# Optimization experiments

Hardware: AMD Instinct MI355X
Metric: run time of the kernel (lower is better)

The kernel has to match this reference:

```python
import jax, jax.numpy as jnp
import numpy as np

O_DIM, A_DIM, Z_DIM = 256, 8, 9
D, H, L, M, B = 128, 128, 4, 4, 65536  # module dim, MLP hidden, n_layers, n_modules, batch


def setup_inputs() -> dict:
    key = jax.random.key(0)
    ks = jax.random.split(key, 18)
    s = 0.05
    return {
        "o": jax.random.normal(ks[0], (B, O_DIM), jnp.float32),
        "z_map": jax.random.uniform(ks[1], (B, Z_DIM), jnp.float32),
        "collision_prob": jax.random.uniform(ks[2], (B, 1), jnp.float32),
        # base obs embedding and routing (task) embedding
        "Wb": jax.random.normal(ks[3], (O_DIM, D), jnp.float32) * s,
        "bb": jnp.zeros((D,), jnp.float32),
        "Wz": jax.random.normal(ks[4], (Z_DIM + 1, D), jnp.float32) * s,
        "bz": jnp.zeros((D,), jnp.float32),
        # L layers x M modules of DxD linears
        "Wm": jax.random.normal(ks[5], (L, M, D, D), jnp.float32) * s,
        "bm": jnp.zeros((L, M, D), jnp.float32),
        # routing heads: L-1 inter-layer (M*M) gates + final (M,) gate
        "Wg": jax.random.normal(ks[6], (L - 1, D, M * M), jnp.float32) * s,
        "Wg_last": jax.random.normal(ks[7], (D, M), jnp.float32) * s,
        # dueling heads
        "Wv": jax.random.normal(ks[8], (D, 1), jnp.float32) * s,
        "bv": jnp.zeros((1,), jnp.float32),
        "Wa1": jax.random.normal(ks[9], (D, H), jnp.float32) * s,
        "ba1": jnp.zeros((H,), jnp.float32),
        "Wa2": jax.random.normal(ks[10], (H, A_DIM), jnp.float32) * s,
        "ba2": jnp.zeros((A_DIM,), jnp.float32),
    }


def _softmodule(o, z_map, collision_prob, Wb, bb, Wz, bz, Wm, bm, Wg, Wg_last):
    f0 = jax.nn.relu(o @ Wb + bb)                              # (B, D)
    z_in = jnp.concatenate([z_map, collision_prob], axis=-1)   # (B, Z+1)
    g = jax.nn.relu(z_in @ Wz + bz) * f0                       # routing embedding (B, D)
    # layer 0: all modules consume the obs embedding
    x = jax.nn.relu(jnp.einsum("bd,mde->bme", f0, Wm[0]) + bm[0])  # (B, M, D)
    for l in range(1, L):
        logits = (g @ Wg[l - 1]).reshape(-1, M, M)             # (B, i, j)
        p = jax.nn.softmax(logits, axis=1)                     # soft routing over incoming modules i
        xin = jnp.einsum("bij,bid->bjd", p, x)                 # weighted gather-combine
        x = jax.nn.relu(jnp.einsum("bmd,mde->bme", xin, Wm[l]) + bm[l])
    p_last = jax.nn.softmax(g @ Wg_last, axis=-1)              # (B, M)
    return jnp.einsum("bm,bmd->bd", p_last, x)                 # (B, D)


def reference(o, z_map, collision_prob, Wb, bb, Wz, bz, Wm, bm, Wg, Wg_last,
              Wv, bv, Wa1, ba1, Wa2, ba2):
    feature = _softmodule(o, z_map, collision_prob, Wb, bb, Wz, bz, Wm, bm, Wg, Wg_last)
    value = feature @ Wv + bv                                  # (B, 1)
    adv = jax.nn.relu(feature @ Wa1 + ba1) @ Wa2 + ba2         # (B, A)
    adv = adv - adv.mean(axis=-1, keepdims=True)
    return adv + value
```

## Files before the change

### kernel.cpp

```cpp
#include <hip/hip_runtime.h>
#include <stdint.h>


typedef __attribute__((ext_vector_type(8))) short short8;
typedef __attribute__((ext_vector_type(4))) float f32x4;
typedef __attribute__((ext_vector_type(2))) float f32x2;
typedef __attribute__((address_space(1))) const unsigned int u32_g;
typedef __attribute__((address_space(3))) unsigned int u32_l;

__device__ __forceinline__ unsigned short f2bf(float f) {
  union { float f; uint32_t u; } v; v.f = f;
  uint32_t r = v.u + 0x7FFFu + ((v.u >> 16) & 1u);
  return (unsigned short)(r >> 16);
}
__device__ __forceinline__ float blo(uint32_t w) { union { uint32_t u; float f; } c; c.u = w << 16; return c.f; }
__device__ __forceinline__ float bhi(uint32_t w) { union { uint32_t u; float f; } c; c.u = w & 0xffff0000u; return c.f; }
__device__ __forceinline__ float b2f(unsigned short h) { union { uint32_t u; float f; } c; c.u = ((uint32_t)h) << 16; return c.f; }
__device__ __forceinline__ uint32_t packrne(float lo, float hi) {
  union { float f; uint32_t u; } a, b; a.f = lo; b.f = hi;
  uint32_t ra = a.u + 0x7fffu + ((a.u >> 16) & 1u);
  uint32_t rb = b.u + 0x7fffu + ((b.u >> 16) & 1u);
  return (ra >> 16) | (rb & 0xffff0000u);
}
__device__ __forceinline__ f32x2 unpk2(uint32_t w) {
  f32x2 r; r.x = blo(w); r.y = bhi(w); return r;
}
union S8 { short8 s; uint32_t u[4]; };

__global__ void prep_weights(const float* __restrict__ Wb, const float* __restrict__ Wm,
                             const float* __restrict__ Wa1, const float* __restrict__ Wg,
                             const float* __restrict__ Wgl, const float* __restrict__ Wa2,
                             unsigned short* __restrict__ ws) {
  int idx = blockIdx.x * 256 + threadIdx.x;
  if (idx >= 321536) return;
  unsigned short v;
  if (idx < 32768) {
    int st = idx >> 12, n = (idx >> 5) & 127, kk = idx & 31;
    v = f2bf(Wb[(st * 32 + kk) * 128 + n]);
  } else if (idx < 40960) {
    int t = idx - 32768; int st = t >> 11, n = (t >> 5) & 63, kk = t & 31;
    int k = st * 32 + kk;
    if (n < 48)      v = f2bf(Wg[(n >> 4) * 2048 + k * 16 + (n & 15)]);
    else if (n < 52) v = f2bf(Wgl[k * 4 + (n - 48)]);
    else             v = 0;
  } else if (idx < 303104) {
    int t = idx - 40960; int lj = t >> 14; int g = t & 16383;
    int st = g >> 12, n = (g >> 5) & 127, kk = g & 31;
    v = f2bf(Wm[lj * 16384 + (st * 32 + kk) * 128 + n]);
  } else if (idx < 319488) {
    int t = idx - 303104; int st = t >> 12, n = (t >> 5) & 127, kk = t & 31;
    v = f2bf(Wa1[(st * 32 + kk) * 128 + n]);
  } else {
    int t = idx - 319488; int st = t >> 9, n = (t >> 5) & 15, kk = t & 31;
    v = (n < 8) ? f2bf(Wa2[(st * 32 + kk) * 8 + n]) : (unsigned short)0;
  }
  ws[idx] = v;
}

__device__ __forceinline__ void gld16(const void* g, void* l) {
  __builtin_amdgcn_global_load_lds((u32_g*)g, (u32_l*)l, 16, 0, 0);
}

__device__ __forceinline__ void gemm32(const short8 xst, const unsigned short* C,
                                       int q, int ml, f32x4 a[8]) {
#pragma unroll
  for (int nt = 0; nt < 8; ++nt) {
    short8 bf = *(const short8*)(C + (nt * 16 + ml) * 32 + q * 8);
    a[nt] = __builtin_amdgcn_mfma_f32_16x16x32_bf16(xst, bf, a[nt], 0, 0, 0);
  }
}

__device__ __forceinline__ void combine_layer(const short8 xo[4][4],
                                              const unsigned short* __restrict__ prow,
                                              short8 xin[4][4]) {
  float p[4][4];
#pragma unroll
  for (int j = 0; j < 4; ++j) {
    uint32_t pw0 = *(const uint32_t*)(prow + j * 4);
    uint32_t pw1 = *(const uint32_t*)(prow + j * 4 + 2);
    p[j][0] = blo(pw0); p[j][1] = bhi(pw0); p[j][2] = blo(pw1); p[j][3] = bhi(pw1);
  }
#pragma unroll
  for (int st = 0; st < 4; ++st) {
    S8 x0, x1, x2, x3;
    x0.s = xo[0][st]; x1.s = xo[1][st]; x2.s = xo[2][st]; x3.s = xo[3][st];
    S8 r0, r1, r2, r3;
#pragma unroll
    for (int w = 0; w < 4; ++w) {
      f32x2 u0 = unpk2(x0.u[w]), u1 = unpk2(x1.u[w]), u2 = unpk2(x2.u[w]), u3 = unpk2(x3.u[w]);
      f32x2 s0 = p[0][0] * u0 + p[0][1] * u1 + p[0][2] * u2 + p[0][3] * u3;
      f32x2 s1 = p[1][0] * u0 + p[1][1] * u1 + p[1][2] * u2 + p[1][3] * u3;
      f32x2 s2 = p[2][0] * u0 + p[2][1] * u1 + p[2][2] * u2 + p[2][3] * u3;
      f32x2 s3 = p[3][0] * u0 + p[3][1] * u1 + p[3][2] * u2 + p[3][3] * u3;
      r0.u[w] = packrne(s0.x, s0.y); r1.u[w] = packrne(s1.x, s1.y);
      r2.u[w] = packrne(s2.x, s2.y); r3.u[w] = packrne(s3.x, s3.y);
    }
    xin[0][st] = r0.s; xin[1][st] = r1.s; xin[2][st] = r2.s; xin[3][st] = r3.s;
  }
}

#define RSYNC1() asm volatile("s_waitcnt vmcnt(1) lgkmcnt(0)\n\ts_barrier" ::: "memory")
#define RSYNC0() asm volatile("s_waitcnt vmcnt(0) lgkmcnt(0)\n\ts_barrier" ::: "memory")
#define RSTEP1(PTR) do { RSYNC1(); ring_issue(); (PTR) = ring_next(); } while (0)
#define RSTEP0(PTR) do { RSYNC0(); ring_issue(); (PTR) = ring_next(); } while (0)

__global__ __attribute__((amdgpu_flat_work_group_size(512, 512), amdgpu_waves_per_eu(4)))
void dueling_fused(
    const float* __restrict__ o, const float* __restrict__ zmap, const float* __restrict__ coll,
    const float* __restrict__ bb, const float* __restrict__ Wz, const float* __restrict__ bz,
    const float* __restrict__ bm, const float* __restrict__ Wv, const float* __restrict__ bv,
    const float* __restrict__ ba1, const float* __restrict__ ba2,
    const unsigned short* __restrict__ ws, float* __restrict__ out)
{
  __shared__ __align__(16) unsigned char smem[77824];
  unsigned short* xbuf  = (unsigned short*)(smem + 24576);
  unsigned short* pall  = (unsigned short*)(smem + 59392);
  float*          zbufF = (float*)(smem + 59392);
  float*          plast = (float*)(smem + 71680);
  float*          vbuf  = (float*)(smem + 71680);
  unsigned short* bmL   = (unsigned short*)(smem + 73728);

  const int tid = threadIdx.x;
  const int wv  = tid >> 6;
  const int lane = tid & 63;
  const int q   = lane >> 4;
  const int ml  = lane & 15;
  const int row0 = blockIdx.x * 128;
  unsigned short* xbw = xbuf + wv * 2176;

  for (int i = tid; i < 1280; i += 512) {
    if (i < 1152) { int r = i / 9, c = i - r * 9; zbufF[r * 12 + c] = zmap[(row0 + r) * 9 + c]; }
    else          { int r = i - 1152; zbufF[r * 12 + 9] = coll[row0 + r]; }
  }
  for (int i = tid; i < 2048; i += 512) bmL[i] = f2bf(bm[i]);

  short8 of[8];
  const float* orow = o + (size_t)(row0 + wv * 16 + ml) * 256;
#pragma unroll
  for (int st = 0; st < 8; ++st) {
    float4 v0 = *(const float4*)(orow + st * 32 + q * 8);
    float4 v1 = *(const float4*)(orow + st * 32 + q * 8 + 4);
    S8 af;
    af.u[0] = packrne(v0.x, v0.y); af.u[1] = packrne(v0.z, v0.w);
    af.u[2] = packrne(v1.x, v1.y); af.u[3] = packrne(v1.z, v1.w);
    of[st] = af.s;
  }
  asm volatile("s_waitcnt vmcnt(0) lgkmcnt(0)" ::: "memory");

  int r_kiss = 0, r_riss = 0, r_rc = 0;
  const char* r_gsrc = (const char*)ws;
  const int wld  = wv << 10;
  const int ln16 = (tid & 63) << 4;
  auto ring_issue = [&]() {
    if (r_kiss <= 78) {
      char* l = (char*)smem + r_riss;
      int soff = (r_kiss == 78) ? (wld & 4095) : wld;
      gld16(r_gsrc + soff + ln16, l + wld + ln16);
      r_gsrc += 8192;
    }
    ++r_kiss;
    r_riss += 8192; if (r_riss == 24576) r_riss = 0;
  };
  auto ring_next = [&]() -> const unsigned short* {
    const unsigned short* p = (const unsigned short*)(smem + r_rc);
    r_rc += 8192; if (r_rc == 24576) r_rc = 0;
    return p;
  };
  ring_issue(); ring_issue();

  const f32x4 z4 = {0.f, 0.f, 0.f, 0.f};
  const unsigned short* C;

  f32x4 acc[8];
#pragma unroll
  for (int nt = 0; nt < 8; ++nt) acc[nt] = z4;
#pragma unroll
  for (int st = 0; st < 8; ++st) { RSTEP1(C); gemm32(of[st], C, q, ml, acc); }
#pragma unroll
  for (int nt = 0; nt < 8; ++nt) {
    float bbv = bb[nt * 16 + ml];
#pragma unroll
    for (int r2 = 0; r2 < 4; ++r2) {
      float v = fmaxf(acc[nt][r2] + bbv, 0.f);
      acc[nt][r2] = v;
      xbw[(q * 4 + r2) * 136 + nt * 16 + ml] = f2bf(v);
    }
  }
  short8 f0f[4];
#pragma unroll
  for (int st = 0; st < 4; ++st) f0f[st] = *(const short8*)(xbw + ml * 136 + st * 32 + q * 8);

#pragma unroll
  for (int nt = 0; nt < 8; ++nt) {
    int col = nt * 16 + ml;
    float wz[10];
#pragma unroll
    for (int k = 0; k < 10; ++k) wz[k] = Wz[k * 128 + col];
    float bzv = bz[col];
#pragma unroll
    for (int r2 = 0; r2 < 4; ++r2) {
      int row = wv * 16 + q * 4 + r2;
      float zd = bzv;
#pragma unroll
      for (int k = 0; k < 10; ++k) zd += zbufF[row * 12 + k] * wz[k];
      xbw[(q * 4 + r2) * 136 + col] = f2bf(fmaxf(zd, 0.f) * acc[nt][r2]);
    }
  }
  short8 gf[4];
#pragma unroll
  for (int st = 0; st < 4; ++st) gf[st] = *(const short8*)(xbw + ml * 136 + st * 32 + q * 8);

#pragma unroll
  for (int nt = 0; nt < 4; ++nt) acc[nt] = z4;
  RSTEP0(C);
#pragma unroll
  for (int sp = 0; sp < 2; ++sp)
#pragma unroll
    for (int nt = 0; nt < 4; ++nt) {
      short8 bf = *(const short8*)(C + (sp * 64 + nt * 16 + ml) * 32 + q * 8);
      acc[nt] = __builtin_amdgcn_mfma_f32_16x16x32_bf16(gf[sp], bf, acc[nt], 0, 0, 0);
    }
  RSTEP1(C);
#pragma unroll
  for (int sp = 0; sp < 2; ++sp)
#pragma unroll
    for (int nt = 0; nt < 4; ++nt) {
      short8 bf = *(const short8*)(C + (sp * 64 + nt * 16 + ml) * 32 + q * 8);
      acc[nt] = __builtin_amdgcn_mfma_f32_16x16x32_bf16(gf[2 + sp], bf, acc[nt], 0, 0, 0);
    }
#pragma unroll
  for (int li = 0; li < 3; ++li) {
#pragma unroll
    for (int r2 = 0; r2 < 4; ++r2) {
      float a = acc[li][r2];
      float m = fmaxf(a, __shfl_xor(a, 4)); m = fmaxf(m, __shfl_xor(m, 8));
      float e = __expf(a - m);
      float s = e; s += __shfl_xor(s, 4); s += __shfl_xor(s, 8);
      pall[(li * 128 + wv * 16 + q * 4 + r2) * 16 + (ml & 3) * 4 + (ml >> 2)] = f2bf(e / s);
    }
  }
#pragma unroll
  for (int r2 = 0; r2 < 4; ++r2) {
    float a = acc[3][r2];
    float m = fmaxf(a, __shfl_xor(a, 1)); m = fmaxf(m, __shfl_xor(m, 2));
    float e = __expf(a - m);
    float s = e; s += __shfl_xor(s, 1); s += __shfl_xor(s, 2);
    if (ml < 4) plast[(wv * 16 + q * 4 + r2) * 4 + ml] = e / s;
  }

  short8 xo[4][4];
  f32x4 a[8];
#pragma unroll
  for (int j = 0; j < 4; ++j) {
    if (j > 0) {
#pragma unroll
      for (int st = 0; st < 4; ++st) xo[j - 1][st] = *(const short8*)(xbw + ml * 136 + st * 32 + q * 8);
    }
#pragma unroll
    for (int nt = 0; nt < 8; ++nt) a[nt] = z4;
#pragma unroll
    for (int st = 0; st < 4; ++st) { RSTEP1(C); gemm32(f0f[st], C, q, ml, a); }
#pragma unroll
    for (int nt = 0; nt < 8; ++nt) {
      float bmv = b2f(bmL[j * 128 + nt * 16 + ml]);
#pragma unroll
      for (int r2 = 0; r2 < 4; ++r2)
        xbw[(q * 4 + r2) * 136 + nt * 16 + ml] = f2bf(fmaxf(a[nt][r2] + bmv, 0.f));
    }
  }

  short8 xin[4][4];
  for (int l = 1; l <= 2; ++l) {
#pragma unroll
    for (int st = 0; st < 4; ++st) xo[3][st] = *(const short8*)(xbw + ml * 136 + st * 32 + q * 8);
    combine_layer(xo, pall + ((l - 1) * 128 + wv * 16 + ml) * 16, xin);
#pragma unroll
    for (int j = 0; j < 4; ++j) {
      if (j > 0) {
#pragma unroll
        for (int st = 0; st < 4; ++st) xo[j - 1][st] = *(const short8*)(xbw + ml * 136 + st * 32 + q * 8);
      }
#pragma unroll
      for (int nt = 0; nt < 8; ++nt) a[nt] = z4;
#pragma unroll
      for (int st = 0; st < 4; ++st) { RSTEP1(C); gemm32(xin[j][st], C, q, ml, a); }
#pragma unroll
      for (int nt = 0; nt < 8; ++nt) {
        float bmv = b2f(bmL[(l * 4 + j) * 128 + nt * 16 + ml]);
#pragma unroll
        for (int r2 = 0; r2 < 4; ++r2)
          xbw[(q * 4 + r2) * 136 + nt * 16 + ml] = f2bf(fmaxf(a[nt][r2] + bmv, 0.f));
      }
    }
  }

  f32x4 feat[8];
  {
#pragma unroll
    for (int st = 0; st < 4; ++st) xo[3][st] = *(const short8*)(xbw + ml * 136 + st * 32 + q * 8);
    combine_layer(xo, pall + (2 * 128 + wv * 16 + ml) * 16, xin);
#pragma unroll
    for (int nt = 0; nt < 8; ++nt) feat[nt] = z4;
#pragma unroll
    for (int j = 0; j < 4; ++j) {
#pragma unroll
      for (int nt = 0; nt < 8; ++nt) a[nt] = z4;
#pragma unroll
      for (int st = 0; st < 4; ++st) { RSTEP1(C); gemm32(xin[j][st], C, q, ml, a); }
      float pl[4];
#pragma unroll
      for (int r2 = 0; r2 < 4; ++r2) pl[r2] = plast[(wv * 16 + q * 4 + r2) * 4 + j];
#pragma unroll
      for (int nt = 0; nt < 8; ++nt) {
        float bmv = b2f(bmL[(12 + j) * 128 + nt * 16 + ml]);
#pragma unroll
        for (int r2 = 0; r2 < 4; ++r2)
          feat[nt][r2] += pl[r2] * fmaxf(a[nt][r2] + bmv, 0.f);
      }
    }
  }

#pragma unroll
  for (int nt = 0; nt < 8; ++nt)
#pragma unroll
    for (int r2 = 0; r2 < 4; ++r2)
      xbw[(q * 4 + r2) * 136 + nt * 16 + ml] = f2bf(feat[nt][r2]);
  short8 ff[4];
#pragma unroll
  for (int st = 0; st < 4; ++st) ff[st] = *(const short8*)(xbw + ml * 136 + st * 32 + q * 8);
#pragma unroll
  for (int nt = 0; nt < 8; ++nt) a[nt] = z4;
#pragma unroll
  for (int st = 0; st < 4; ++st) { RSTEP1(C); gemm32(ff[st], C, q, ml, a); }

  {
    float wvv[8];
#pragma unroll
    for (int nt = 0; nt < 8; ++nt) wvv[nt] = Wv[nt * 16 + ml];
    float bvv = bv[0];
#pragma unroll
    for (int r2 = 0; r2 < 4; ++r2) {
      float v = 0.f;
#pragma unroll
      for (int nt = 0; nt < 8; ++nt) v += feat[nt][r2] * wvv[nt];
      v += __shfl_xor(v, 1); v += __shfl_xor(v, 2); v += __shfl_xor(v, 4); v += __shfl_xor(v, 8);
      if (ml == 0) vbuf[wv * 16 + q * 4 + r2] = v + bvv;
    }
  }

#pragma unroll
  for (int nt = 0; nt < 8; ++nt) {
    float b1v = ba1[nt * 16 + ml];
#pragma unroll
    for (int r2 = 0; r2 < 4; ++r2)
      xbw[(q * 4 + r2) * 136 + nt * 16 + ml] = f2bf(fmaxf(a[nt][r2] + b1v, 0.f));
  }
  short8 a1f[4];
#pragma unroll
  for (int st = 0; st < 4; ++st) a1f[st] = *(const short8*)(xbw + ml * 136 + st * 32 + q * 8);

  RSTEP0(C);
  f32x4 av = z4;
#pragma unroll
  for (int st = 0; st < 4; ++st) {
    short8 bf = *(const short8*)(C + (st * 16 + ml) * 32 + q * 8);
    av = __builtin_amdgcn_mfma_f32_16x16x32_bf16(a1f[st], bf, av, 0, 0, 0);
  }
  float ba2v = ba2[ml & 7];
#pragma unroll
  for (int r2 = 0; r2 < 4; ++r2) {
    float aa = av[r2] + ba2v;
    float s = aa + __shfl_xor(aa, 1); s += __shfl_xor(s, 2); s += __shfl_xor(s, 4);
    if (ml < 8)
      out[(size_t)(row0 + wv * 16 + q * 4 + r2) * 8 + ml] = aa - s * 0.125f + vbuf[wv * 16 + q * 4 + r2];
  }
}

extern "C" void kernel_launch(void* const* d_in, const int* in_sizes, int n_in,
                              void* d_out, int out_size, void* d_ws, size_t ws_size,
                              hipStream_t stream) {
  const float* o   = (const float*)d_in[0];
  const float* zm  = (const float*)d_in[1];
  const float* cp  = (const float*)d_in[2];
  const float* Wb  = (const float*)d_in[3];
  const float* bb  = (const float*)d_in[4];
  const float* Wz  = (const float*)d_in[5];
  const float* bz  = (const float*)d_in[6];
  const float* Wm  = (const float*)d_in[7];
  const float* bm  = (const float*)d_in[8];
  const float* Wg  = (const float*)d_in[9];
  const float* Wgl = (const float*)d_in[10];
  const float* Wv  = (const float*)d_in[11];
  const float* bv  = (const float*)d_in[12];
  const float* Wa1 = (const float*)d_in[13];
  const float* ba1 = (const float*)d_in[14];
  const float* Wa2 = (const float*)d_in[15];
  const float* ba2 = (const float*)d_in[16];
  unsigned short* wsT = (unsigned short*)d_ws;

  int B = in_sizes[0] / 256;

  hipLaunchKernelGGL(prep_weights, dim3(1256), dim3(256), 0, stream,
                     Wb, Wm, Wa1, Wg, Wgl, Wa2, wsT);
  hipLaunchKernelGGL(dueling_fused, dim3(B / 128), dim3(512), 0, stream,
                     o, zm, cp, bb, Wz, bz, bm, Wv, bv, ba1, ba2,
                     wsT, (float*)d_out);
}
```

Baseline: 223.9 us.

## Process two 16-row tiles per wave to reuse each weight fragment twice

Each wave now handles 32 rows instead of 16, so every B-fragment loaded from the LDS weight ring feeds two MFMAs, and the block tile grows to 256 rows. The weight staging layout is rearranged so each lane's 8-element k-slice is contiguous per q group, which changes the LDS read pattern. The intent is to halve the weight streaming and ring barriers per row and cut LDS traffic per MFMA. In exchange it uses more registers and LDS (waves_per_eu lowered to 2, shared memory about 124KB), which reduces occupancy, and launches half as many blocks.

Result: no change. 226.2 us (+1.0%).

```diff
diff --git a/kernel.cpp b/kernel.cpp
--- a/kernel.cpp
+++ b/kernel.cpp
@@ -35,24 +35,25 @@
   if (idx >= 321536) return;
   unsigned short v;
   if (idx < 32768) {
-    int st = idx >> 12, n = (idx >> 5) & 127, kk = idx & 31;
-    v = f2bf(Wb[(st * 32 + kk) * 128 + n]);
+    int st = idx >> 12, q = (idx >> 10) & 3, n = (idx >> 3) & 127, kk = idx & 7;
+    v = f2bf(Wb[(st * 32 + q * 8 + kk) * 128 + n]);
   } else if (idx < 40960) {
-    int t = idx - 32768; int st = t >> 11, n = (t >> 5) & 63, kk = t & 31;
-    int k = st * 32 + kk;
+    int t = idx - 32768; int st = t >> 11, q = (t >> 9) & 3, n = (t >> 3) & 63, kk = t & 7;
+    int k = st * 32 + q * 8 + kk;
     if (n < 48)      v = f2bf(Wg[(n >> 4) * 2048 + k * 16 + (n & 15)]);
     else if (n < 52) v = f2bf(Wgl[k * 4 + (n - 48)]);
     else             v = 0;
   } else if (idx < 303104) {
-    int t = idx - 40960; int lj = t >> 14; int g = t & 16383;
-    int st = g >> 12, n = (g >> 5) & 127, kk = g & 31;
-    v = f2bf(Wm[lj * 16384 + (st * 32 + kk) * 128 + n]);
+    int t = idx - 40960; int pg = t >> 12; int lj = pg >> 2, st = pg & 3;
+    int q = (t >> 10) & 3, n = (t >> 3) & 127, kk = t & 7;
+    v = f2bf(Wm[lj * 16384 + (st * 32 + q * 8 + kk) * 128 + n]);
   } else if (idx < 319488) {
-    int t = idx - 303104; int st = t >> 12, n = (t >> 5) & 127, kk = t & 31;
-    v = f2bf(Wa1[(st * 32 + kk) * 128 + n]);
+    int t = idx - 303104; int st = t >> 12, q = (t >> 10) & 3, n = (t >> 3) & 127, kk = t & 7;
+    v = f2bf(Wa1[(st * 32 + q * 8 + kk) * 128 + n]);
   } else {
-    int t = idx - 319488; int st = t >> 9, n = (t >> 5) & 15, kk = t & 31;
-    v = (n < 8) ? f2bf(Wa2[(st * 32 + kk) * 8 + n]) : (unsigned short)0;
+    int t = idx - 319488; int st = t >> 9, q = (t >> 7) & 3, n = (t >> 3) & 15, kk = t & 7;
+    int k = st * 32 + q * 8 + kk;
+    v = (n < 8) ? f2bf(Wa2[k * 8 + n]) : (unsigned short)0;
   }
   ws[idx] = v;
 }
@@ -61,13 +62,22 @@
   __builtin_amdgcn_global_load_lds((u32_g*)g, (u32_l*)l, 16, 0, 0);
 }
 
-__device__ __forceinline__ void gemm32(const short8 xst, const unsigned short* C,
-                                       int q, int ml, f32x4 a[8]) {
+__device__ __forceinline__ void ldb8(const unsigned short* C, int q, int ml, short8 bf[8]) {
+#pragma unroll
+  for (int nt = 0; nt < 8; ++nt)
+    bf[nt] = *(const short8*)(C + q * 1024 + (nt * 16 + ml) * 8);
+}
+__device__ __forceinline__ void mfma2x8(const short8 x0, const short8 x1, const short8 bf[8],
+                                        f32x4 a0[8], f32x4 a1[8]) {
 #pragma unroll
   for (int nt = 0; nt < 8; ++nt) {
-    short8 bf = *(const short8*)(C + (nt * 16 + ml) * 32 + q * 8);
-    a[nt] = __builtin_amdgcn_mfma_f32_16x16x32_bf16(xst, bf, a[nt], 0, 0, 0);
-  }
+    a0[nt] = __builtin_amdgcn_mfma_f32_16x16x32_bf16(x0, bf[nt], a0[nt], 0, 0, 0);
+    a1[nt] = __builtin_amdgcn_mfma_f32_16x16x32_bf16(x1, bf[nt], a1[nt], 0, 0, 0);
+  }
+}
+__device__ __forceinline__ void ldx4(const unsigned short* xbw, int q, int ml, short8 f[4]) {
+#pragma unroll
+  for (int st = 0; st < 4; ++st) f[st] = *(const short8*)(xbw + ml * 136 + st * 32 + q * 8);
 }
 
 __device__ __forceinline__ void combine_layer(const short8 xo[4][4],
@@ -104,7 +114,7 @@
 #define RSTEP1(PTR) do { RSYNC1(); ring_issue(); (PTR) = ring_next(); } while (0)
 #define RSTEP0(PTR) do { RSYNC0(); ring_issue(); (PTR) = ring_next(); } while (0)
 
-__global__ __attribute__((amdgpu_flat_work_group_size(512, 512), amdgpu_waves_per_eu(4)))
+__global__ __attribute__((amdgpu_flat_work_group_size(512, 512), amdgpu_waves_per_eu(2)))
 void dueling_fused(
     const float* __restrict__ o, const float* __restrict__ zmap, const float* __restrict__ coll,
     const float* __restrict__ bb, const float* __restrict__ Wz, const float* __restrict__ bz,
@@ -112,38 +122,41 @@
     const float* __restrict__ ba1, const float* __restrict__ ba2,
     const unsigned short* __restrict__ ws, float* __restrict__ out)
 {
-  __shared__ __align__(16) unsigned char smem[77824];
+  __shared__ __align__(16) unsigned char smem[126976];
   unsigned short* xbuf  = (unsigned short*)(smem + 24576);
-  unsigned short* pall  = (unsigned short*)(smem + 59392);
-  float*          zbufF = (float*)(smem + 59392);
-  float*          plast = (float*)(smem + 71680);
-  float*          vbuf  = (float*)(smem + 71680);
-  unsigned short* bmL   = (unsigned short*)(smem + 73728);
+  unsigned short* pall  = (unsigned short*)(smem + 94208);
+  float*          zbufF = (float*)(smem + 94208);
+  float*          plast = (float*)(smem + 118784);
+  float*          vbuf  = (float*)(smem + 118784);
+  unsigned short* bmL   = (unsigned short*)(smem + 122880);
 
   const int tid = threadIdx.x;
   const int wv  = tid >> 6;
   const int lane = tid & 63;
   const int q   = lane >> 4;
   const int ml  = lane & 15;
-  const int row0 = blockIdx.x * 128;
-  unsigned short* xbw = xbuf + wv * 2176;
-
-  for (int i = tid; i < 1280; i += 512) {
-    if (i < 1152) { int r = i / 9, c = i - r * 9; zbufF[r * 12 + c] = zmap[(row0 + r) * 9 + c]; }
-    else          { int r = i - 1152; zbufF[r * 12 + 9] = coll[row0 + r]; }
+  const int row0 = blockIdx.x * 256;
+  unsigned short* xbwA[2] = { xbuf + wv * 4352, xbuf + wv * 4352 + 2176 };
+
+  for (int i = tid; i < 2560; i += 512) {
+    if (i < 2304) { int r = i / 9, c = i - r * 9; zbufF[r * 12 + c] = zmap[(row0 + r) * 9 + c]; }
+    else          { int r = i - 2304; zbufF[r * 12 + 9] = coll[row0 + r]; }
   }
   for (int i = tid; i < 2048; i += 512) bmL[i] = f2bf(bm[i]);
 
-  short8 of[8];
-  const float* orow = o + (size_t)(row0 + wv * 16 + ml) * 256;
-#pragma unroll
-  for (int st = 0; st < 8; ++st) {
-    float4 v0 = *(const float4*)(orow + st * 32 + q * 8);
-    float4 v1 = *(const float4*)(orow + st * 32 + q * 8 + 4);
-    S8 af;
-    af.u[0] = packrne(v0.x, v0.y); af.u[1] = packrne(v0.z, v0.w);
-    af.u[2] = packrne(v1.x, v1.y); af.u[3] = packrne(v1.z, v1.w);
-    of[st] = af.s;
+  short8 of[2][8];
+#pragma unroll
+  for (int rs = 0; rs < 2; ++rs) {
+    const float* orow = o + (size_t)(row0 + wv * 32 + rs * 16 + ml) * 256;
+#pragma unroll
+    for (int st = 0; st < 8; ++st) {
+      float4 v0 = *(const float4*)(orow + st * 32 + q * 8);
+      float4 v1 = *(const float4*)(orow + st * 32 + q * 8 + 4);
+      S8 af;
+      af.u[0] = packrne(v0.x, v0.y); af.u[1] = packrne(v0.z, v0.w);
+      af.u[2] = packrne(v1.x, v1.y); af.u[3] = packrne(v1.z, v1.w);
+      of[rs][st] = af.s;
+    }
   }
   asm volatile("s_waitcnt vmcnt(0) lgkmcnt(0)" ::: "memory");
 
@@ -171,24 +184,31 @@
   const f32x4 z4 = {0.f, 0.f, 0.f, 0.f};
   const unsigned short* C;
 
-  f32x4 acc[8];
-#pragma unroll
-  for (int nt = 0; nt < 8; ++nt) acc[nt] = z4;
-#pragma unroll
-  for (int st = 0; st < 8; ++st) { RSTEP1(C); gemm32(of[st], C, q, ml, acc); }
+  f32x4 acc[2][8];
+#pragma unroll
+  for (int rs = 0; rs < 2; ++rs)
+#pragma unroll
+    for (int nt = 0; nt < 8; ++nt) acc[rs][nt] = z4;
+#pragma unroll
+  for (int st = 0; st < 8; ++st) {
+    RSTEP1(C);
+    short8 bf[8]; ldb8(C, q, ml, bf);
+    mfma2x8(of[0][st], of[1][st], bf, acc[0], acc[1]);
+  }
 #pragma unroll
   for (int nt = 0; nt < 8; ++nt) {
     float bbv = bb[nt * 16 + ml];
 #pragma unroll
-    for (int r2 = 0; r2 < 4; ++r2) {
-      float v = fmaxf(acc[nt][r2] + bbv, 0.f);
-      acc[nt][r2] = v;
-      xbw[(q * 4 + r2) * 136 + nt * 16 + ml] = f2bf(v);
-    }
-  }
-  short8 f0f[4];
-#pragma unroll
-  for (int st = 0; st < 4; ++st) f0f[st] = *(const short8*)(xbw + ml * 136 + st * 32 + q * 8);
+    for (int rs = 0; rs < 2; ++rs)
+#pragma unroll
+      for (int r2 = 0; r2 < 4; ++r2) {
+        float v = fmaxf(acc[rs][nt][r2] + bbv, 0.f);
+        acc[rs][nt][r2] = v;
+        xbwA[rs][(q * 4 + r2) * 136 + nt * 16 + ml] = f2bf(v);
+      }
+  }
+  short8 f0f[2][4];
+  ldx4(xbwA[0], q, ml, f0f[0]); ldx4(xbwA[1], q, ml, f0f[1]);
 
 #pragma unroll
   for (int nt = 0; nt < 8; ++nt) {
@@ -198,182 +218,226 @@
     for (int k = 0; k < 10; ++k) wz[k] = Wz[k * 128 + col];
     float bzv = bz[col];
 #pragma unroll
+    for (int rs = 0; rs < 2; ++rs)
+#pragma unroll
+      for (int r2 = 0; r2 < 4; ++r2) {
+        int row = wv * 32 + rs * 16 + q * 4 + r2;
+        float zd = bzv;
+#pragma unroll
+        for (int k = 0; k < 10; ++k) zd += zbufF[row * 12 + k] * wz[k];
+        xbwA[rs][(q * 4 + r2) * 136 + col] = f2bf(fmaxf(zd, 0.f) * acc[rs][nt][r2]);
+      }
+  }
+  short8 gf[2][4];
+  ldx4(xbwA[0], q, ml, gf[0]); ldx4(xbwA[1], q, ml, gf[1]);
+
+  f32x4 ag[2][4];
+#pragma unroll
+  for (int rs = 0; rs < 2; ++rs)
+#pragma unroll
+    for (int nt = 0; nt < 4; ++nt) ag[rs][nt] = z4;
+  RSTEP0(C);
+#pragma unroll
+  for (int sp = 0; sp < 2; ++sp)
+#pragma unroll
+    for (int nt = 0; nt < 4; ++nt) {
+      short8 bf = *(const short8*)(C + sp * 2048 + q * 512 + (nt * 16 + ml) * 8);
+      ag[0][nt] = __builtin_amdgcn_mfma_f32_16x16x32_bf16(gf[0][sp], bf, ag[0][nt], 0, 0, 0);
+      ag[1][nt] = __builtin_amdgcn_mfma_f32_16x16x32_bf16(gf[1][sp], bf, ag[1][nt], 0, 0, 0);
+    }
+  RSTEP1(C);
+#pragma unroll
+  for (int sp = 0; sp < 2; ++sp)
+#pragma unroll
+    for (int nt = 0; nt < 4; ++nt) {
+      short8 bf = *(const short8*)(C + sp * 2048 + q * 512 + (nt * 16 + ml) * 8);
+      ag[0][nt] = __builtin_amdgcn_mfma_f32_16x16x32_bf16(gf[0][2 + sp], bf, ag[0][nt], 0, 0, 0);
+      ag[1][nt] = __builtin_amdgcn_mfma_f32_16x16x32_bf16(gf[1][2 + sp], bf, ag[1][nt], 0, 0, 0);
+    }
+#pragma unroll
+  for (int rs = 0; rs < 2; ++rs) {
+#pragma unroll
+    for (int li = 0; li < 3; ++li) {
+#pragma unroll
+      for (int r2 = 0; r2 < 4; ++r2) {
+        float a = ag[rs][li][r2];
+        float m = fmaxf(a, __shfl_xor(a, 4)); m = fmaxf(m, __shfl_xor(m, 8));
+        float e = __expf(a - m);
+        float s = e; s += __shfl_xor(s, 4); s += __shfl_xor(s, 8);
+        pall[(li * 256 + wv * 32 + rs * 16 + q * 4 + r2) * 16 + (ml & 3) * 4 + (ml >> 2)] = f2bf(e / s);
+      }
+    }
+#pragma unroll
     for (int r2 = 0; r2 < 4; ++r2) {
-      int row = wv * 16 + q * 4 + r2;
-      float zd = bzv;
-#pragma unroll
-      for (int k = 0; k < 10; ++k) zd += zbufF[row * 12 + k] * wz[k];
-      xbw[(q * 4 + r2) * 136 + col] = f2bf(fmaxf(zd, 0.f) * acc[nt][r2]);
-    }
-  }
-  short8 gf[4];
-#pragma unroll
-  for (int st = 0; st < 4; ++st) gf[st] = *(const short8*)(xbw + ml * 136 + st * 32 + q * 8);
-
-#pragma unroll
-  for (int nt = 0; nt < 4; ++nt) acc[nt] = z4;
-  RSTEP0(C);
-#pragma unroll
-  for (int sp = 0; sp < 2; ++sp)
-#pragma unroll
-    for (int nt = 0; nt < 4; ++nt) {
-      short8 bf = *(const short8*)(C + (sp * 64 + nt * 16 + ml) * 32 + q * 8);
-      acc[nt] = __builtin_amdgcn_mfma_f32_16x16x32_bf16(gf[sp], bf, acc[nt], 0, 0, 0);
-    }
-  RSTEP1(C);
-#pragma unroll
-  for (int sp = 0; sp < 2; ++sp)
-#pragma unroll
-    for (int nt = 0; nt < 4; ++nt) {
-      short8 bf = *(const short8*)(C + (sp * 64 + nt * 16 + ml) * 32 + q * 8);
-      acc[nt] = __builtin_amdgcn_mfma_f32_16x16x32_bf16(gf[2 + sp], bf, acc[nt], 0, 0, 0);
-    }
-#pragma unroll
-  for (int li = 0; li < 3; ++li) {
-#pragma unroll
-    for (int r2 = 0; r2 < 4; ++r2) {
-      float a = acc[li][r2];
-      float m = fmaxf(a, __shfl_xor(a, 4)); m = fmaxf(m, __shfl_xor(m, 8));
+      float a = ag[rs][3][r2];
+      float m = fmaxf(a, __shfl_xor(a, 1)); m = fmaxf(m, __shfl_xor(m, 2));
       float e = __expf(a - m);
-      float s = e; s += __shfl_xor(s, 4); s += __shfl_xor(s, 8);
-      pall[(li * 128 + wv * 16 + q * 4 + r2) * 16 + (ml & 3) * 4 + (ml >> 2)] = f2bf(e / s);
-    }
-  }
-#pragma unroll
-  for (int r2 = 0; r2 < 4; ++r2) {
-    float a = acc[3][r2];
-    float m = fmaxf(a, __shfl_xor(a, 1)); m = fmaxf(m, __shfl_xor(m, 2));
-    float e = __expf(a - m);
-    float s = e; s += __shfl_xor(s, 1); s += __shfl_xor(s, 2);
-    if (ml < 4) plast[(wv * 16 + q * 4 + r2) * 4 + ml] = e / s;
-  }
-
-  short8 xo[4][4];
-  f32x4 a[8];
+      float s = e; s += __shfl_xor(s, 1); s += __shfl_xor(s, 2);
+      if (ml < 4) plast[(wv * 32 + rs * 16 + q * 4 + r2) * 4 + ml] = e / s;
+    }
+  }
+
+  short8 xo[2][4][4];
+  f32x4 a2[2][8];
 #pragma unroll
   for (int j = 0; j < 4; ++j) {
-    if (j > 0) {
-#pragma unroll
-      for (int st = 0; st < 4; ++st) xo[j - 1][st] = *(const short8*)(xbw + ml * 136 + st * 32 + q * 8);
-    }
-#pragma unroll
-    for (int nt = 0; nt < 8; ++nt) a[nt] = z4;
-#pragma unroll
-    for (int st = 0; st < 4; ++st) { RSTEP1(C); gemm32(f0f[st], C, q, ml, a); }
+    if (j > 0) { ldx4(xbwA[0], q, ml, xo[0][j - 1]); ldx4(xbwA[1], q, ml, xo[1][j - 1]); }
+#pragma unroll
+    for (int rs = 0; rs < 2; ++rs)
+#pragma unroll
+      for (int nt = 0; nt < 8; ++nt) a2[rs][nt] = z4;
+#pragma unroll
+    for (int st = 0; st < 4; ++st) {
+      RSTEP1(C);
+      short8 bf[8]; ldb8(C, q, ml, bf);
+      mfma2x8(f0f[0][st], f0f[1][st], bf, a2[0], a2[1]);
+    }
 #pragma unroll
     for (int nt = 0; nt < 8; ++nt) {
       float bmv = b2f(bmL[j * 128 + nt * 16 + ml]);
 #pragma unroll
-      for (int r2 = 0; r2 < 4; ++r2)
-        xbw[(q * 4 + r2) * 136 + nt * 16 + ml] = f2bf(fmaxf(a[nt][r2] + bmv, 0.f));
-    }
-  }
-
-  short8 xin[4][4];
+      for (int rs = 0; rs < 2; ++rs)
+#pragma unroll
+        for (int r2 = 0; r2 < 4; ++r2)
+          xbwA[rs][(q * 4 + r2) * 136 + nt * 16 + ml] = f2bf(fmaxf(a2[rs][nt][r2] + bmv, 0.f));
+    }
+  }
+
+  short8 xin[2][4][4];
   for (int l = 1; l <= 2; ++l) {
-#pragma unroll
-    for (int st = 0; st < 4; ++st) xo[3][st] = *(const short8*)(xbw + ml * 136 + st * 32 + q * 8);
-    combine_layer(xo, pall + ((l - 1) * 128 + wv * 16 + ml) * 16, xin);
+    ldx4(xbwA[0], q, ml, xo[0][3]);
+    combine_layer(xo[0], pall + ((l - 1) * 256 + wv * 32 + ml) * 16, xin[0]);
+    ldx4(xbwA[1], q, ml, xo[1][3]);
+    combine_layer(xo[1], pall + ((l - 1) * 256 + wv * 32 + 16 + ml) * 16, xin[1]);
 #pragma unroll
     for (int j = 0; j < 4; ++j) {
-      if (j > 0) {
-#pragma unroll
-        for (int st = 0; st < 4; ++st) xo[j - 1][st] = *(const short8*)(xbw + ml * 136 + st * 32 + q * 8);
-      }
-#pragma unroll
-      for (int nt = 0; nt < 8; ++nt) a[nt] = z4;
-#pragma unroll
-      for (int st = 0; st < 4; ++st) { RSTEP1(C); gemm32(xin[j][st], C, q, ml, a); }
+      if (j > 0) { ldx4(xbwA[0], q, ml, xo[0][j - 1]); ldx4(xbwA[1], q, ml, xo[1][j - 1]); }
+#pragma unroll
+      for (int rs = 0; rs < 2; ++rs)
+#pragma unroll
+        for (int nt = 0; nt < 8; ++nt) a2[rs][nt] = z4;
+#pragma unroll
+      for (int st = 0; st < 4; ++st) {
+        RSTEP1(C);
+        short8 bf[8]; ldb8(C, q, ml, bf);
+        mfma2x8(xin[0][j][st], xin[1][j][st], bf, a2[0], a2[1]);
+      }
 #pragma unroll
       for (int nt = 0; nt < 8; ++nt) {
         float bmv = b2f(bmL[(l * 4 + j) * 128 + nt * 16 + ml]);
 #pragma unroll
-        for (int r2 = 0; r2 < 4; ++r2)
-          xbw[(q * 4 + r2) * 136 + nt * 16 + ml] = f2bf(fmaxf(a[nt][r2] + bmv, 0.f));
-      }
-    }
-  }
-
-  f32x4 feat[8];
+        for (int rs = 0; rs < 2; ++rs)
+#pragma unroll
+          for (int r2 = 0; r2 < 4; ++r2)
+            xbwA[rs][(q * 4 + r2) * 136 + nt * 16 + ml] = f2bf(fmaxf(a2[rs][nt][r2] + bmv, 0.f));
+      }
+    }
+  }
+
+  f32x4 feat[2][8];
   {
-#pragma unroll
-    for (int st = 0; st < 4; ++st) xo[3][st] = *(const short8*)(xbw + ml * 136 + st * 32 + q * 8);
-    combine_layer(xo, pall + (2 * 128 + wv * 16 + ml) * 16, xin);
-#pragma unroll
-    for (int nt = 0; nt < 8; ++nt) feat[nt] = z4;
+    ldx4(xbwA[0], q, ml, xo[0][3]);
+    combine_layer(xo[0], pall + (2 * 256 + wv * 32 + ml) * 16, xin[0]);
+    ldx4(xbwA[1], q, ml, xo[1][3]);
+    combine_layer(xo[1], pall + (2 * 256 + wv * 32 + 16 + ml) * 16, xin[1]);
+#pragma unroll
+    for (int rs = 0; rs < 2; ++rs)
+#pragma unroll
+      for (int nt = 0; nt < 8; ++nt) feat[rs][nt] = z4;
 #pragma unroll
     for (int j = 0; j < 4; ++j) {
 #pragma unroll
-      for (int nt = 0; nt < 8; ++nt) a[nt] = z4;
-#pragma unroll
-      for (int st = 0; st < 4; ++st) { RSTEP1(C); gemm32(xin[j][st], C, q, ml, a); }
-      float pl[4];
-#pragma unroll
-      for (int r2 = 0; r2 < 4; ++r2) pl[r2] = plast[(wv * 16 + q * 4 + r2) * 4 + j];
-#pragma unroll
-      for (int nt = 0; nt < 8; ++nt) {
-        float bmv = b2f(bmL[(12 + j) * 128 + nt * 16 + ml]);
-#pragma unroll
-        for (int r2 = 0; r2 < 4; ++r2)
-          feat[nt][r2] += pl[r2] * fmaxf(a[nt][r2] + bmv, 0.f);
-      }
-    }
-  }
-
-#pragma unroll
-  for (int nt = 0; nt < 8; ++nt)
-#pragma unroll
-    for (int r2 = 0; r2 < 4; ++r2)
-      xbw[(q * 4 + r2) * 136 + nt * 16 + ml] = f2bf(feat[nt][r2]);
-  short8 ff[4];
-#pragma unroll
-  for (int st = 0; st < 4; ++st) ff[st] = *(const short8*)(xbw + ml * 136 + st * 32 + q * 8);
-#pragma unroll
-  for (int nt = 0; nt < 8; ++nt) a[nt] = z4;
-#pragma unroll
-  for (int st = 0; st < 4; ++st) { RSTEP1(C); gemm32(ff[st], C, q, ml, a); }
-
+      for (int rs = 0; rs < 2; ++rs)
+#pragma unroll
+        for (int nt = 0; nt < 8; ++nt) a2[rs][nt] = z4;
+#pragma unroll
+      for (int st = 0; st < 4; ++st) {
+        RSTEP1(C);
+        short8 bf[8]; ldb8(C, q, ml, bf);
+        mfma2x8(xin[0][j][st], xin[1][j][st], bf, a2[0], a2[1]);
+      }
+#pragma unroll
+      for (int rs = 0; rs < 2; ++rs) {
+        float pl[4];
+#pragma unroll
+        for (int r2 = 0; r2 < 4; ++r2) pl[r2] = plast[(wv * 32 + rs * 16 + q * 4 + r2) * 4 + j];
+#pragma unroll
+        for (int nt = 0; nt < 8; ++nt) {
+          float bmv = b2f(bmL[(12 + j) * 128 + nt * 16 + ml]);
+#pragma unroll
+          for (int r2 = 0; r2 < 4; ++r2)
+            feat[rs][nt][r2] += pl[r2] * fmaxf(a2[rs][nt][r2] + bmv, 0.f);
+        }
+      }
+    }
+  }
+
+#pragma unroll
+  for (int rs = 0; rs < 2; ++rs)
+#pragma unroll
+    for (int nt = 0; nt < 8; ++nt)
+#pragma unroll
+      for (int r2 = 0; r2 < 4; ++r2)
+        xbwA[rs][(q * 4 + r2) * 136 + nt * 16 + ml] = f2bf(feat[rs][nt][r2]);
   {
     float wvv[8];
 #pragma unroll
     for (int nt = 0; nt < 8; ++nt) wvv[nt] = Wv[nt * 16 + ml];
     float bvv = bv[0];
 #pragma unroll
-    for (int r2 = 0; r2 < 4; ++r2) {
-      float v = 0.f;
-#pragma unroll
-      for (int nt = 0; nt < 8; ++nt) v += feat[nt][r2] * wvv[nt];
-      v += __shfl_xor(v, 1); v += __shfl_xor(v, 2); v += __shfl_xor(v, 4); v += __shfl_xor(v, 8);
-      if (ml == 0) vbuf[wv * 16 + q * 4 + r2] = v + bvv;
-    }
-  }
-
+    for (int rs = 0; rs < 2; ++rs)
+#pragma unroll
+      for (int r2 = 0; r2 < 4; ++r2) {
+        float v = 0.f;
+#pragma unroll
+        for (int nt = 0; nt < 8; ++nt) v += feat[rs][nt][r2] * wvv[nt];
+        v += __shfl_xor(v, 1); v += __shfl_xor(v, 2); v += __shfl_xor(v, 4); v += __shfl_xor(v, 8);
+        if (ml == 0) vbuf[wv * 32 + rs * 16 + q * 4 + r2] = v + bvv;
+      }
+  }
+  short8 ff[2][4];
+  ldx4(xbwA[0], q, ml, ff[0]); ldx4(xbwA[1], q, ml, ff[1]);
+#pragma unroll
+  for (int rs = 0; rs < 2; ++rs)
+#pragma unroll
+    for (int nt = 0; nt < 8; ++nt) a2[rs][nt] = z4;
+#pragma unroll
+  for (int st = 0; st < 4; ++st) {
+    RSTEP1(C);
+    short8 bf[8]; ldb8(C, q, ml, bf);
+    mfma2x8(ff[0][st], ff[1][st], bf, a2[0], a2[1]);
+  }
 #pragma unroll
   for (int nt = 0; nt < 8; ++nt) {
     float b1v = ba1[nt * 16 + ml];
 #pragma unroll
-    for (int r2 = 0; r2 < 4; ++r2)
-      xbw[(q * 4 + r2) * 136 + nt * 16 + ml] = f2bf(fmaxf(a[nt][r2] + b1v, 0.f));
-  }
-  short8 a1f[4];
-#pragma unroll
-  for (int st = 0; st < 4; ++st) a1f[st] = *(const short8*)(xbw + ml * 136 + st * 32 + q * 8);
+    for (int rs = 0; rs < 2; ++rs)
+#pragma unroll
+      for (int r2 = 0; r2 < 4; ++r2)
+        xbwA[rs][(q * 4 + r2) * 136 + nt * 16 + ml] = f2bf(fmaxf(a2[rs][nt][r2] + b1v, 0.f));
+  }
+  short8 a1f[2][4];
+  ldx4(xbwA[0], q, ml, a1f[0]); ldx4(xbwA[1], q, ml, a1f[1]);
 
   RSTEP0(C);
-  f32x4 av = z4;
+  f32x4 av[2] = { z4, z4 };
 #pragma unroll
   for (int st = 0; st < 4; ++st) {
-    short8 bf = *(const short8*)(C + (st * 16 + ml) * 32 + q * 8);
-    av = __builtin_amdgcn_mfma_f32_16x16x32_bf16(a1f[st], bf, av, 0, 0, 0);
+    short8 bf = *(const short8*)(C + st * 512 + q * 128 + ml * 8);
+    av[0] = __builtin_amdgcn_mfma_f32_16x16x32_bf16(a1f[0][st], bf, av[0], 0, 0, 0);
+    av[1] = __builtin_amdgcn_mfma_f32_16x16x32_bf16(a1f[1][st], bf, av[1], 0, 0, 0);
   }
   float ba2v = ba2[ml & 7];
 #pragma unroll
-  for (int r2 = 0; r2 < 4; ++r2) {
-    float aa = av[r2] + ba2v;
-    float s = aa + __shfl_xor(aa, 1); s += __shfl_xor(s, 2); s += __shfl_xor(s, 4);
-    if (ml < 8)
-      out[(size_t)(row0 + wv * 16 + q * 4 + r2) * 8 + ml] = aa - s * 0.125f + vbuf[wv * 16 + q * 4 + r2];
-  }
+  for (int rs = 0; rs < 2; ++rs)
+#pragma unroll
+    for (int r2 = 0; r2 < 4; ++r2) {
+      float aa = av[rs][r2] + ba2v;
+      float s = aa + __shfl_xor(aa, 1); s += __shfl_xor(s, 2); s += __shfl_xor(s, 4);
+      if (ml < 8)
+        out[(size_t)(row0 + wv * 32 + rs * 16 + q * 4 + r2) * 8 + ml] =
+            aa - s * 0.125f + vbuf[wv * 32 + rs * 16 + q * 4 + r2];
+    }
 }
 
 extern "C" void kernel_launch(void* const* d_in, const int* in_sizes, int n_in,
@@ -402,7 +466,7 @@
 
   hipLaunchKernelGGL(prep_weights, dim3(1256), dim3(256), 0, stream,
                      Wb, Wm, Wa1, Wg, Wgl, Wa2, wsT);
-  hipLaunchKernelGGL(dueling_fused, dim3(B / 128), dim3(512), 0, stream,
+  hipLaunchKernelGGL(dueling_fused, dim3(B / 256), dim3(512), 0, stream,
                      o, zm, cp, bb, Wz, bz, bm, Wv, bv, ba1, ba2,
                      wsT, (float*)d_out);
 }
```
